# Performance work log

Measured on AMD Instinct MI355X. Metric: run time of the kernel, lower is better.

The kernel has to match this reference:

```python
import jax, jax.numpy as jnp
import numpy as np

B, T, F, H, O = 8192, 10, 561, 256, 12


def _lstm_cell(x, h, c, Wih, Whh, bih, bhh):
    # PyTorch gate order: input, forget, cell(g), output
    gates = x @ Wih.T + bih + h @ Whh.T + bhh  # [B, 4H]
    i, f, g, o = jnp.split(gates, 4, axis=-1)
    c_new = jax.nn.sigmoid(f) * c + jax.nn.sigmoid(i) * jnp.tanh(g)
    h_new = jax.nn.sigmoid(o) * jnp.tanh(c_new)
    return h_new, c_new


def setup_inputs() -> dict:
    key = jax.random.key(0)
    ks = jax.random.split(key, 12)
    s_in = 1.0 / np.sqrt(F)
    s_h = 1.0 / np.sqrt(H)
    u = lambda k, shape, s: jax.random.uniform(k, shape, jnp.float32, -s, s)
    return {
        "inputs": jax.random.normal(ks[0], (B, T, F), jnp.float32),
        "W_inp": u(ks[1], (H, F), s_in), "b_inp": u(ks[2], (H,), s_in),
        "Wih0": u(ks[3], (4 * H, H), s_h), "Whh0": u(ks[4], (4 * H, H), s_h),
        "bih0": u(ks[5], (4 * H,), s_h), "bhh0": u(ks[6], (4 * H,), s_h),
        "Wih1": u(ks[7], (4 * H, H), s_h), "Whh1": u(ks[8], (4 * H, H), s_h),
        "bih1": u(ks[9], (4 * H,), s_h), "bhh1": u(ks[10], (4 * H,), s_h),
        "W_out": u(ks[11], (O, H), s_h), "b_out": jnp.zeros((O,), jnp.float32),
    }


def reference(inputs, W_inp, b_inp, Wih0, Whh0, bih0, bhh0,
              Wih1, Whh1, bih1, bhh1, W_out, b_out):
    b, t, _ = inputs.shape
    h = W_inp.shape[0]
    # input Linear applied to every timestep (same math as per-step self.inp)
    xp = jnp.einsum('btf,hf->bth', inputs, W_inp) + b_inp  # [B,T,H]

    def step(carry, x_t):
        h0, c0, h1, c1 = carry
        h0, c0 = _lstm_cell(x_t, h0, c0, Wih0, Whh0, bih0, bhh0)
        h1, c1 = _lstm_cell(h0, h1, c1, Wih1, Whh1, bih1, bhh1)
        return (h0, c0, h1, c1), h1

    z = jnp.zeros((b, h), inputs.dtype)
    (h0, c0, h1, c1), hs = jax.lax.scan(step, (z, z, z, z), jnp.swapaxes(xp, 0, 1))
    outputs = jnp.einsum('tbh,oh->bto', hs, W_out) + b_out  # [B,T,O]
    h_n = jnp.stack([h0, h1])  # [2,B,H] like torch LSTM hidden
    c_n = jnp.stack([c0, c1])
    return outputs, h_n, c_n
```

## Files before the change

kernel.cpp:

```cpp
#include <hip/hip_runtime.h>

#define BB 8192
#define TT 10
#define FF 561
#define FP 576
#define HH 256
#define OO 12

typedef __attribute__((ext_vector_type(8))) __bf16 bf16x8;
typedef __attribute__((ext_vector_type(4))) float f32x4;

__device__ __forceinline__ unsigned short f2bf(float f) {
  unsigned int u = __float_as_uint(f);
  u += 0x7fffu + ((u >> 16) & 1u);
  return (unsigned short)(u >> 16);
}
__device__ __forceinline__ float bf2f(unsigned short s) {
  return __uint_as_float(((unsigned int)s) << 16);
}
__device__ __forceinline__ float sigm(float x) { return 1.f / (1.f + __expf(-x)); }
__device__ __forceinline__ float tanh_fast(float x) { return 1.f - 2.f / (__expf(2.f * x) + 1.f); }

__device__ __forceinline__ void gl_lds16(const unsigned short* g, unsigned short* l) {
  __builtin_amdgcn_global_load_lds(
      (const __attribute__((address_space(1))) unsigned int*)g,
      (__attribute__((address_space(3))) unsigned int*)l, 16, 0, 0);
}

__global__ void conv_inputs(const float* __restrict__ in, unsigned short* __restrict__ Ain) {
  int idx = blockIdx.x * 256 + threadIdx.x;
  if (idx >= 81920 * 144) return;
  int c4 = (idx % 144) * 4;
  size_t row = idx / 144;
  const float* src = in + row * 561 + c4;
  ushort4 v;
  v.x = f2bf(c4 + 0 < 561 ? src[0] : 0.f);
  v.y = f2bf(c4 + 1 < 561 ? src[1] : 0.f);
  v.z = f2bf(c4 + 2 < 561 ? src[2] : 0.f);
  v.w = f2bf(c4 + 3 < 561 ? src[3] : 0.f);
  *(ushort4*)(Ain + row * 576 + c4) = v;
}

__global__ void conv_weights(const float* __restrict__ Winp,
                             const float* __restrict__ Wih0, const float* __restrict__ Whh0,
                             const float* __restrict__ Wih1, const float* __restrict__ Whh1,
                             const float* __restrict__ Wout,
                             unsigned short* __restrict__ Wib,
                             unsigned short* __restrict__ W0p,
                             unsigned short* __restrict__ W1p,
                             unsigned short* __restrict__ Wob) {
  int idx = blockIdx.x * 256 + threadIdx.x;
  if (idx < 256 * 576) {
    int kk = idx % 576, n = idx / 576;
    Wib[idx] = f2bf(kk < 561 ? Winp[n * 561 + kk] : 0.f);
    return;
  }
  idx -= 256 * 576;
  if (idx < 1024 * 512) {
    int kk = idx % 512, np = idx / 512;
    int h = (np >> 7) * 32 + (np & 31), g = (np >> 5) & 3;
    int sr = g * 256 + h;
    float v = kk < 256 ? Wih0[sr * 256 + kk] : Whh0[sr * 256 + kk - 256];
    W0p[idx] = f2bf(v);
    return;
  }
  idx -= 1024 * 512;
  if (idx < 1024 * 512) {
    int kk = idx % 512, np = idx / 512;
    int h = (np >> 7) * 32 + (np & 31), g = (np >> 5) & 3;
    int sr = g * 256 + h;
    float v = kk < 256 ? Wih1[sr * 256 + kk] : Whh1[sr * 256 + kk - 256];
    W1p[idx] = f2bf(v);
    return;
  }
  idx -= 1024 * 512;
  if (idx < 16 * 256) {
    int kk = idx % 256, o = idx / 256;
    Wob[idx] = f2bf(o < OO ? Wout[o * 256 + kk] : 0.f);
  }
}

template <int MODE>
__global__ __launch_bounds__(256, 2) void gemm_k(
    const unsigned short* __restrict__ A0, int lda0, int K0,
    const unsigned short* __restrict__ A1, int lda1,
    const unsigned short* __restrict__ W, int K,
    const float* __restrict__ biasA, const float* __restrict__ biasB,
    float* __restrict__ cbuf,
    unsigned short* __restrict__ hout,
    float* __restrict__ hf32, float* __restrict__ cf32) {
  __shared__ __align__(16) unsigned short As[2][128 * 32];
  __shared__ __align__(16) unsigned short Bs[2][128 * 32];
  const int tid = threadIdx.x;
  const int w = tid >> 6, lane = tid & 63, quad = lane >> 4, l15 = lane & 15;
  const int mb = blockIdx.x, nb = blockIdx.y;

  f32x4 acc[2][8];
#pragma unroll
  for (int i = 0; i < 2; ++i)
#pragma unroll
    for (int j = 0; j < 8; ++j) acc[i][j] = (f32x4){0.f, 0.f, 0.f, 0.f};

  const int r0 = tid >> 2;
  const int cc = (tid & 3) * 8;

  auto stage = [&](int k0, int buf) {
    const unsigned short* Asrc;
    int ldA, kk;
    if (k0 < K0) { Asrc = A0; ldA = lda0; kk = k0; }
    else         { Asrc = A1; ldA = lda1; kk = k0 - K0; }
    gl_lds16(Asrc + (size_t)(mb * 128 + r0) * ldA + kk + cc, &As[buf][tid * 8]);
    gl_lds16(Asrc + (size_t)(mb * 128 + 64 + r0) * ldA + kk + cc, &As[buf][2048 + tid * 8]);
    gl_lds16(W + (size_t)(nb * 128 + r0) * K + k0 + cc, &Bs[buf][tid * 8]);
    gl_lds16(W + (size_t)(nb * 128 + 64 + r0) * K + k0 + cc, &Bs[buf][2048 + tid * 8]);
  };

  stage(0, 0);
  __syncthreads();

  int p = 0;
  for (int k0 = 0; k0 < K; k0 += 32) {
    if (k0 + 32 < K) stage(k0 + 32, p ^ 1);

    bf16x8 af[2], bfr[8];
#pragma unroll
    for (int mt = 0; mt < 2; ++mt)
      af[mt] = *(const bf16x8*)&As[p][(w * 32 + mt * 16 + l15) * 32 + quad * 8];
#pragma unroll
    for (int nt = 0; nt < 8; ++nt)
      bfr[nt] = *(const bf16x8*)&Bs[p][(nt * 16 + l15) * 32 + quad * 8];
#pragma unroll
    for (int mt = 0; mt < 2; ++mt)
#pragma unroll
      for (int nt = 0; nt < 8; ++nt)
        acc[mt][nt] = __builtin_amdgcn_mfma_f32_16x16x32_bf16(af[mt], bfr[nt], acc[mt][nt], 0, 0, 0);

    __syncthreads();
    p ^= 1;
  }

  if constexpr (MODE == 0) {
#pragma unroll
    for (int mt = 0; mt < 2; ++mt) {
      int rowb = mb * 128 + w * 32 + mt * 16 + quad * 4;
#pragma unroll
      for (int nt = 0; nt < 8; ++nt) {
        int col = nb * 128 + nt * 16 + l15;
        float bv = biasA[col];
#pragma unroll
        for (int r = 0; r < 4; ++r)
          hout[(size_t)(rowb + r) * HH + col] = f2bf(acc[mt][nt][r] + bv);
      }
    }
  } else {
#pragma unroll
    for (int hb = 0; hb < 2; ++hb) {
      int hg = nb * 32 + hb * 16 + l15;
      float bI = biasA[hg] + biasB[hg];
      float bF = biasA[256 + hg] + biasB[256 + hg];
      float bG = biasA[512 + hg] + biasB[512 + hg];
      float bO = biasA[768 + hg] + biasB[768 + hg];
#pragma unroll
      for (int mt = 0; mt < 2; ++mt) {
        int rowb = mb * 128 + w * 32 + mt * 16 + quad * 4;
#pragma unroll
        for (int r = 0; r < 4; ++r) {
          size_t idx = (size_t)(rowb + r) * HH + hg;
          float xi = acc[mt][0 + hb][r] + bI;
          float xf = acc[mt][2 + hb][r] + bF;
          float xg = acc[mt][4 + hb][r] + bG;
          float xo = acc[mt][6 + hb][r] + bO;
          float c_old = cbuf[idx];
          float cn = sigm(xf) * c_old + sigm(xi) * tanh_fast(xg);
          float hn = sigm(xo) * tanh_fast(cn);
          cbuf[idx] = cn;
          hout[idx] = f2bf(hn);
          if (hf32) hf32[idx] = hn;
          if (cf32) cf32[idx] = cn;
        }
      }
    }
  }
}

__global__ __launch_bounds__(256) void out_gemm_mfma(
    const unsigned short* __restrict__ hs,
    const unsigned short* __restrict__ Wob,
    const float* __restrict__ bout,
    float* __restrict__ out) {
  const int tid = threadIdx.x;
  const int w = tid >> 6, lane = tid & 63, quad = lane >> 4, l15 = lane & 15;
  const int m0 = blockIdx.x * 64 + w * 16;
  const unsigned short* arow = hs + (size_t)(m0 + l15 + BB) * HH + quad * 8;
  const unsigned short* brow = Wob + l15 * HH + quad * 8;
  f32x4 acc = (f32x4){0.f, 0.f, 0.f, 0.f};
#pragma unroll
  for (int k0 = 0; k0 < 8; ++k0) {
    bf16x8 a = *(const bf16x8*)(arow + k0 * 32);
    bf16x8 b = *(const bf16x8*)(brow + k0 * 32);
    acc = __builtin_amdgcn_mfma_f32_16x16x32_bf16(a, b, acc, 0, 0, 0);
  }
  const int o = l15;
  if (o < OO) {
    float bv = bout[o];
#pragma unroll
    for (int r = 0; r < 4; ++r) {
      int m = m0 + quad * 4 + r;
      int b = m & (BB - 1);
      int t = m >> 13;
      out[((size_t)b * TT + t) * OO + o] = acc[r] + bv;
    }
  }
}

extern "C" void kernel_launch(void* const* d_in, const int* in_sizes, int n_in,
                              void* d_out, int out_size, void* d_ws, size_t ws_size,
                              hipStream_t stream) {
  const float* inputs = (const float*)d_in[0];
  const float* W_inp  = (const float*)d_in[1];
  const float* b_inp  = (const float*)d_in[2];
  const float* Wih0   = (const float*)d_in[3];
  const float* Whh0   = (const float*)d_in[4];
  const float* bih0   = (const float*)d_in[5];
  const float* bhh0   = (const float*)d_in[6];
  const float* Wih1   = (const float*)d_in[7];
  const float* Whh1   = (const float*)d_in[8];
  const float* bih1   = (const float*)d_in[9];
  const float* bhh1   = (const float*)d_in[10];
  const float* W_out  = (const float*)d_in[11];
  const float* b_out  = (const float*)d_in[12];
  float* out = (float*)d_out;

  char* ws = (char*)d_ws;
  size_t off = 0;
  auto alloc = [&](size_t bytes) {
    char* p = ws + off;
    off += (bytes + 255) & ~(size_t)255;
    return p;
  };
  unsigned short* Ain = (unsigned short*)alloc((size_t)81920 * FP * 2);
  unsigned short* xp  = (unsigned short*)alloc((size_t)81920 * HH * 2);
  unsigned short* Wib = (unsigned short*)alloc((size_t)256 * FP * 2);
  unsigned short* W0p = (unsigned short*)alloc((size_t)1024 * 512 * 2);
  unsigned short* W1p = (unsigned short*)alloc((size_t)1024 * 512 * 2);
  unsigned short* Wob = (unsigned short*)alloc((size_t)16 * HH * 2);
  unsigned short* h0s = (unsigned short*)alloc((size_t)2 * BB * HH * 2);
  unsigned short* hs  = (unsigned short*)alloc((size_t)(TT + 1) * BB * HH * 2);
  float* c0 = (float*)alloc((size_t)BB * HH * 4);
  float* c1 = (float*)alloc((size_t)BB * HH * 4);

  hipMemsetAsync(h0s, 0, (size_t)BB * HH * 2, stream);
  hipMemsetAsync(hs, 0, (size_t)BB * HH * 2, stream);
  hipMemsetAsync(c0, 0, (size_t)BB * HH * 4, stream);
  hipMemsetAsync(c1, 0, (size_t)BB * HH * 4, stream);

  conv_inputs<<<(81920 * 144 + 255) / 256, 256, 0, stream>>>(inputs, Ain);
  {
    int nthr = 256 * 576 + 2 * 1024 * 512 + 16 * 256;
    conv_weights<<<(nthr + 255) / 256, 256, 0, stream>>>(W_inp, Wih0, Whh0, Wih1, Whh1,
                                                         W_out, Wib, W0p, W1p, Wob);
  }

  gemm_k<0><<<dim3(640, 2), 256, 0, stream>>>(
      Ain, FP, FP, (const unsigned short*)nullptr, 0,
      Wib, FP, b_inp, (const float*)nullptr,
      (float*)nullptr, xp, (float*)nullptr, (float*)nullptr);

  float* hn_out = out + (size_t)BB * TT * OO;
  float* cn_out = hn_out + (size_t)2 * BB * HH;

  for (int t = 0; t < TT; ++t) {
    const unsigned short* h0_prev = h0s + (size_t)(t & 1) * BB * HH;
    unsigned short* h0_new       = h0s + (size_t)((t + 1) & 1) * BB * HH;
    const unsigned short* xpt = xp + (size_t)t * HH;
    const unsigned short* h1_prev = hs + (size_t)t * BB * HH;
    unsigned short* h1_new        = hs + (size_t)(t + 1) * BB * HH;
    bool last = (t == TT - 1);

    gemm_k<1><<<dim3(64, 8), 256, 0, stream>>>(
        xpt, TT * HH, 256, h0_prev, HH,
        W0p, 512, bih0, bhh0, c0, h0_new,
        last ? hn_out : (float*)nullptr,
        last ? cn_out : (float*)nullptr);

    gemm_k<1><<<dim3(64, 8), 256, 0, stream>>>(
        h0_new, HH, 256, h1_prev, HH,
        W1p, 512, bih1, bhh1, c1, h1_new,
        last ? hn_out + (size_t)BB * HH : (float*)nullptr,
        last ? cn_out + (size_t)BB * HH : (float*)nullptr);
  }

  out_gemm_mfma<<<1280, 256, 0, stream>>>(hs, Wob, b_out, out);
}
```

Baseline: 790.8 us.

## Fuse LSTM recurrence into persistent cooperative kernel with wavefront layer pipelining

Replaces the 20 per-timestep GEMM launches with a single cooperative persistent kernel of 256 blocks. Half the blocks run layer 0 and half run layer 1, skewed by one step so both layers compute concurrently, with a grid sync between phases. The input projection now reads fp32 inputs directly through LDS and converts them to bf16 in registers, which removes the separate conversion kernel and its padded bf16 buffer. Tiles grow to 256x256 with 512 threads. The risks are grid-sync overhead, occupancy limits for cooperative launch, and the larger fp32 A tile in LDS.

```diff
diff --git a/kernel.cpp b/kernel.cpp
--- a/kernel.cpp
+++ b/kernel.cpp
@@ -1,4 +1,7 @@
 #include <hip/hip_runtime.h>
+#include <hip/hip_cooperative_groups.h>
+
+namespace cg = cooperative_groups;
 
 #define BB 8192
 #define TT 10
@@ -15,9 +18,6 @@
   u += 0x7fffu + ((u >> 16) & 1u);
   return (unsigned short)(u >> 16);
 }
-__device__ __forceinline__ float bf2f(unsigned short s) {
-  return __uint_as_float(((unsigned int)s) << 16);
-}
 __device__ __forceinline__ float sigm(float x) { return 1.f / (1.f + __expf(-x)); }
 __device__ __forceinline__ float tanh_fast(float x) { return 1.f - 2.f / (__expf(2.f * x) + 1.f); }
 
@@ -26,19 +26,19 @@
       (const __attribute__((address_space(1))) unsigned int*)g,
       (__attribute__((address_space(3))) unsigned int*)l, 16, 0, 0);
 }
-
-__global__ void conv_inputs(const float* __restrict__ in, unsigned short* __restrict__ Ain) {
-  int idx = blockIdx.x * 256 + threadIdx.x;
-  if (idx >= 81920 * 144) return;
-  int c4 = (idx % 144) * 4;
-  size_t row = idx / 144;
-  const float* src = in + row * 561 + c4;
-  ushort4 v;
-  v.x = f2bf(c4 + 0 < 561 ? src[0] : 0.f);
-  v.y = f2bf(c4 + 1 < 561 ? src[1] : 0.f);
-  v.z = f2bf(c4 + 2 < 561 ? src[2] : 0.f);
-  v.w = f2bf(c4 + 3 < 561 ? src[3] : 0.f);
-  *(ushort4*)(Ain + row * 576 + c4) = v;
+__device__ __forceinline__ void gl_lds4(const float* g, float* l) {
+  __builtin_amdgcn_global_load_lds(
+      (const __attribute__((address_space(1))) unsigned int*)g,
+      (__attribute__((address_space(3))) unsigned int*)l, 4, 0, 0);
+}
+
+__device__ __forceinline__ bf16x8 cvt8(const float* fp) {
+  f32x4 x0 = *(const f32x4*)fp;
+  f32x4 x1 = *(const f32x4*)(fp + 4);
+  union { bf16x8 v; unsigned short s[8]; } u;
+  u.s[0] = f2bf(x0[0]); u.s[1] = f2bf(x0[1]); u.s[2] = f2bf(x0[2]); u.s[3] = f2bf(x0[3]);
+  u.s[4] = f2bf(x1[0]); u.s[5] = f2bf(x1[1]); u.s[6] = f2bf(x1[2]); u.s[7] = f2bf(x1[3]);
+  return u.v;
 }
 
 __global__ void conv_weights(const float* __restrict__ Winp,
@@ -80,105 +80,193 @@
   }
 }
 
-template <int MODE>
-__global__ __launch_bounds__(256, 2) void gemm_k(
-    const unsigned short* __restrict__ A0, int lda0, int K0,
-    const unsigned short* __restrict__ A1, int lda1,
-    const unsigned short* __restrict__ W, int K,
-    const float* __restrict__ biasA, const float* __restrict__ biasB,
-    float* __restrict__ cbuf,
-    unsigned short* __restrict__ hout,
-    float* __restrict__ hf32, float* __restrict__ cf32) {
-  __shared__ __align__(16) unsigned short As[2][128 * 32];
-  __shared__ __align__(16) unsigned short Bs[2][128 * 32];
+__global__ __launch_bounds__(512, 2) void xp_gemm(
+    const float* __restrict__ in,
+    const unsigned short* __restrict__ Wib,
+    const float* __restrict__ binp,
+    unsigned short* __restrict__ xp) {
+  __shared__ __align__(16) float Af[2][128 * 32];
+  __shared__ __align__(16) unsigned short Bs[2][256 * 32];
   const int tid = threadIdx.x;
   const int w = tid >> 6, lane = tid & 63, quad = lane >> 4, l15 = lane & 15;
-  const int mb = blockIdx.x, nb = blockIdx.y;
+  const int wr = w & 3, wc = w >> 2;
+  const int mb = blockIdx.x;
+  const int ar = tid >> 5, acl = tid & 31;
+  const int sr = tid >> 2, sc = (tid & 3) * 8;
+
+  auto stage = [&](int k0, int buf) {
+#pragma unroll
+    for (int ii = 0; ii < 8; ++ii) {
+      int row = mb * 128 + ii * 16 + ar;
+      int col = k0 + acl; col = col < FF ? col : FF - 1;
+      gl_lds4(in + (size_t)row * FF + col, &Af[buf][(ii * 16 + ar) * 32 + acl]);
+    }
+    const unsigned short* g1 = Wib + (size_t)sr * FP + k0 + sc;
+    gl_lds16(g1, &Bs[buf][tid * 8]);
+    gl_lds16(g1 + (size_t)128 * FP, &Bs[buf][4096 + tid * 8]);
+  };
 
   f32x4 acc[2][8];
 #pragma unroll
   for (int i = 0; i < 2; ++i)
 #pragma unroll
     for (int j = 0; j < 8; ++j) acc[i][j] = (f32x4){0.f, 0.f, 0.f, 0.f};
-
-  const int r0 = tid >> 2;
-  const int cc = (tid & 3) * 8;
-
-  auto stage = [&](int k0, int buf) {
-    const unsigned short* Asrc;
-    int ldA, kk;
-    if (k0 < K0) { Asrc = A0; ldA = lda0; kk = k0; }
-    else         { Asrc = A1; ldA = lda1; kk = k0 - K0; }
-    gl_lds16(Asrc + (size_t)(mb * 128 + r0) * ldA + kk + cc, &As[buf][tid * 8]);
-    gl_lds16(Asrc + (size_t)(mb * 128 + 64 + r0) * ldA + kk + cc, &As[buf][2048 + tid * 8]);
-    gl_lds16(W + (size_t)(nb * 128 + r0) * K + k0 + cc, &Bs[buf][tid * 8]);
-    gl_lds16(W + (size_t)(nb * 128 + 64 + r0) * K + k0 + cc, &Bs[buf][2048 + tid * 8]);
-  };
 
   stage(0, 0);
   __syncthreads();
-
-  int p = 0;
-  for (int k0 = 0; k0 < K; k0 += 32) {
-    if (k0 + 32 < K) stage(k0 + 32, p ^ 1);
-
+  int pb = 0;
+  for (int k0 = 0; k0 < FP; k0 += 32) {
+    if (k0 + 32 < FP) stage(k0 + 32, pb ^ 1);
     bf16x8 af[2], bfr[8];
 #pragma unroll
     for (int mt = 0; mt < 2; ++mt)
-      af[mt] = *(const bf16x8*)&As[p][(w * 32 + mt * 16 + l15) * 32 + quad * 8];
+      af[mt] = cvt8(&Af[pb][(wr * 32 + mt * 16 + l15) * 32 + quad * 8]);
 #pragma unroll
     for (int nt = 0; nt < 8; ++nt)
-      bfr[nt] = *(const bf16x8*)&Bs[p][(nt * 16 + l15) * 32 + quad * 8];
+      bfr[nt] = *(const bf16x8*)&Bs[pb][(wc * 128 + nt * 16 + l15) * 32 + quad * 8];
 #pragma unroll
     for (int mt = 0; mt < 2; ++mt)
 #pragma unroll
       for (int nt = 0; nt < 8; ++nt)
         acc[mt][nt] = __builtin_amdgcn_mfma_f32_16x16x32_bf16(af[mt], bfr[nt], acc[mt][nt], 0, 0, 0);
-
     __syncthreads();
-    p ^= 1;
-  }
-
-  if constexpr (MODE == 0) {
-#pragma unroll
-    for (int mt = 0; mt < 2; ++mt) {
-      int rowb = mb * 128 + w * 32 + mt * 16 + quad * 4;
-#pragma unroll
-      for (int nt = 0; nt < 8; ++nt) {
-        int col = nb * 128 + nt * 16 + l15;
-        float bv = biasA[col];
-#pragma unroll
-        for (int r = 0; r < 4; ++r)
-          hout[(size_t)(rowb + r) * HH + col] = f2bf(acc[mt][nt][r] + bv);
+    pb ^= 1;
+  }
+
+#pragma unroll
+  for (int mt = 0; mt < 2; ++mt) {
+    int rowb = mb * 128 + wr * 32 + mt * 16 + quad * 4;
+#pragma unroll
+    for (int nt = 0; nt < 8; ++nt) {
+      int col = wc * 128 + nt * 16 + l15;
+      float bv = binp[col];
+#pragma unroll
+      for (int r = 0; r < 4; ++r)
+        xp[(size_t)(rowb + r) * HH + col] = f2bf(acc[mt][nt][r] + bv);
+    }
+  }
+}
+
+__global__ __launch_bounds__(512, 2) void lstm_recurrence(
+    const unsigned short* __restrict__ xp,
+    const unsigned short* __restrict__ W0p,
+    const unsigned short* __restrict__ W1p,
+    const float* __restrict__ bih0, const float* __restrict__ bhh0,
+    const float* __restrict__ bih1, const float* __restrict__ bhh1,
+    unsigned short* __restrict__ h0s,
+    unsigned short* __restrict__ hs,
+    float* __restrict__ c0, float* __restrict__ c1,
+    float* __restrict__ hn_out, float* __restrict__ cn_out) {
+  __shared__ __align__(16) unsigned short As[2][256 * 32];
+  __shared__ __align__(16) unsigned short Bs[2][256 * 32];
+  cg::grid_group gg = cg::this_grid();
+
+  const int tid = threadIdx.x;
+  const int w = tid >> 6, lane = tid & 63, quad = lane >> 4, l15 = lane & 15;
+  const int wr = w & 3, wc = w >> 2;
+  const int i = blockIdx.x;
+  const int xcd = i & 7, slot = i >> 3;
+  const int group = xcd >> 2;
+  const int mb = (xcd & 3) * 8 + (slot >> 2);
+  const int nb = slot & 3;
+
+  const unsigned short* W = group ? W1p : W0p;
+  const float* bA = group ? bih1 : bih0;
+  const float* bB = group ? bhh1 : bhh0;
+  float* cbuf = group ? c1 : c0;
+
+  const int sr = tid >> 2, sc = (tid & 3) * 8;
+
+  for (int p = 0; p <= TT; ++p) {
+    const bool active = group ? (p >= 1) : (p < TT);
+    if (active) {
+      const int t = group ? p - 1 : p;
+      const unsigned short* A0;
+      int lda0;
+      if (group) { A0 = h0s + (size_t)(p & 1) * BB * HH; lda0 = HH; }
+      else       { A0 = xp + (size_t)t * HH;             lda0 = TT * HH; }
+      const unsigned short* A1 = group ? (hs + (size_t)t * BB * HH)
+                                       : (h0s + (size_t)(p & 1) * BB * HH);
+
+      auto stageA = [&](int k0, int buf) {
+        const unsigned short* Asrc;
+        int ldA, kk;
+        if (k0 < 256) { Asrc = A0; ldA = lda0; kk = k0; }
+        else          { Asrc = A1; ldA = HH;   kk = k0 - 256; }
+        const unsigned short* g0 = Asrc + (size_t)(mb * 256 + sr) * ldA + kk + sc;
+        gl_lds16(g0, &As[buf][tid * 8]);
+        gl_lds16(g0 + (size_t)128 * ldA, &As[buf][4096 + tid * 8]);
+        const unsigned short* g1 = W + (size_t)(nb * 256 + sr) * 512 + k0 + sc;
+        gl_lds16(g1, &Bs[buf][tid * 8]);
+        gl_lds16(g1 + (size_t)128 * 512, &Bs[buf][4096 + tid * 8]);
+      };
+
+      f32x4 acc[4][8];
+#pragma unroll
+      for (int a = 0; a < 4; ++a)
+#pragma unroll
+        for (int b = 0; b < 8; ++b) acc[a][b] = (f32x4){0.f, 0.f, 0.f, 0.f};
+
+      stageA(0, 0);
+      __syncthreads();
+      int pb = 0;
+      for (int k0 = 0; k0 < 512; k0 += 32) {
+        if (k0 + 32 < 512) stageA(k0 + 32, pb ^ 1);
+        bf16x8 af[4], bfr[8];
+#pragma unroll
+        for (int mt = 0; mt < 4; ++mt)
+          af[mt] = *(const bf16x8*)&As[pb][(wr * 64 + mt * 16 + l15) * 32 + quad * 8];
+#pragma unroll
+        for (int nt = 0; nt < 8; ++nt)
+          bfr[nt] = *(const bf16x8*)&Bs[pb][(wc * 128 + nt * 16 + l15) * 32 + quad * 8];
+#pragma unroll
+        for (int mt = 0; mt < 4; ++mt)
+#pragma unroll
+          for (int nt = 0; nt < 8; ++nt)
+            acc[mt][nt] = __builtin_amdgcn_mfma_f32_16x16x32_bf16(af[mt], bfr[nt], acc[mt][nt], 0, 0, 0);
+        __syncthreads();
+        pb ^= 1;
       }
-    }
-  } else {
-#pragma unroll
-    for (int hb = 0; hb < 2; ++hb) {
-      int hg = nb * 32 + hb * 16 + l15;
-      float bI = biasA[hg] + biasB[hg];
-      float bF = biasA[256 + hg] + biasB[256 + hg];
-      float bG = biasA[512 + hg] + biasB[512 + hg];
-      float bO = biasA[768 + hg] + biasB[768 + hg];
-#pragma unroll
-      for (int mt = 0; mt < 2; ++mt) {
-        int rowb = mb * 128 + w * 32 + mt * 16 + quad * 4;
-#pragma unroll
-        for (int r = 0; r < 4; ++r) {
-          size_t idx = (size_t)(rowb + r) * HH + hg;
-          float xi = acc[mt][0 + hb][r] + bI;
-          float xf = acc[mt][2 + hb][r] + bF;
-          float xg = acc[mt][4 + hb][r] + bG;
-          float xo = acc[mt][6 + hb][r] + bO;
-          float c_old = cbuf[idx];
-          float cn = sigm(xf) * c_old + sigm(xi) * tanh_fast(xg);
-          float hn = sigm(xo) * tanh_fast(cn);
-          cbuf[idx] = cn;
-          hout[idx] = f2bf(hn);
-          if (hf32) hf32[idx] = hn;
-          if (cf32) cf32[idx] = cn;
+
+      unsigned short* hout = group ? (hs + (size_t)(t + 1) * BB * HH)
+                                   : (h0s + (size_t)((p + 1) & 1) * BB * HH);
+      float* hf = nullptr; float* cf = nullptr;
+      if (t == TT - 1) {
+        hf = hn_out + (group ? (size_t)BB * HH : 0);
+        cf = cn_out + (group ? (size_t)BB * HH : 0);
+      }
+      const int hg32 = (2 * nb + wc) * 32;
+#pragma unroll
+      for (int hb = 0; hb < 2; ++hb) {
+        const int hgl = hg32 + hb * 16 + l15;
+        float bI = bA[hgl] + bB[hgl];
+        float bF = bA[256 + hgl] + bB[256 + hgl];
+        float bG = bA[512 + hgl] + bB[512 + hgl];
+        float bO = bA[768 + hgl] + bB[768 + hgl];
+#pragma unroll
+        for (int mt = 0; mt < 4; ++mt) {
+          const int rowb = mb * 256 + wr * 64 + mt * 16 + quad * 4;
+#pragma unroll
+          for (int r = 0; r < 4; ++r) {
+            const size_t idx = (size_t)(rowb + r) * HH + hgl;
+            float xi = acc[mt][0 + hb][r] + bI;
+            float xf = acc[mt][2 + hb][r] + bF;
+            float xg = acc[mt][4 + hb][r] + bG;
+            float xo = acc[mt][6 + hb][r] + bO;
+            float c_old = cbuf[idx];
+            float cn = sigm(xf) * c_old + sigm(xi) * tanh_fast(xg);
+            float hn = sigm(xo) * tanh_fast(cn);
+            cbuf[idx] = cn;
+            hout[idx] = f2bf(hn);
+            if (hf) hf[idx] = hn;
+            if (cf) cf[idx] = cn;
+          }
         }
       }
+    }
+    if (p < TT) {
+      __threadfence();
+      gg.sync();
     }
   }
 }
@@ -238,7 +326,6 @@
     off += (bytes + 255) & ~(size_t)255;
     return p;
   };
-  unsigned short* Ain = (unsigned short*)alloc((size_t)81920 * FP * 2);
   unsigned short* xp  = (unsigned short*)alloc((size_t)81920 * HH * 2);
   unsigned short* Wib = (unsigned short*)alloc((size_t)256 * FP * 2);
   unsigned short* W0p = (unsigned short*)alloc((size_t)1024 * 512 * 2);
@@ -254,40 +341,24 @@
   hipMemsetAsync(c0, 0, (size_t)BB * HH * 4, stream);
   hipMemsetAsync(c1, 0, (size_t)BB * HH * 4, stream);
 
-  conv_inputs<<<(81920 * 144 + 255) / 256, 256, 0, stream>>>(inputs, Ain);
   {
     int nthr = 256 * 576 + 2 * 1024 * 512 + 16 * 256;
     conv_weights<<<(nthr + 255) / 256, 256, 0, stream>>>(W_inp, Wih0, Whh0, Wih1, Whh1,
                                                          W_out, Wib, W0p, W1p, Wob);
   }
 
-  gemm_k<0><<<dim3(640, 2), 256, 0, stream>>>(
-      Ain, FP, FP, (const unsigned short*)nullptr, 0,
-      Wib, FP, b_inp, (const float*)nullptr,
-      (float*)nullptr, xp, (float*)nullptr, (float*)nullptr);
+  xp_gemm<<<640, 512, 0, stream>>>(inputs, Wib, b_inp, xp);
 
   float* hn_out = out + (size_t)BB * TT * OO;
   float* cn_out = hn_out + (size_t)2 * BB * HH;
 
-  for (int t = 0; t < TT; ++t) {
-    const unsigned short* h0_prev = h0s + (size_t)(t & 1) * BB * HH;
-    unsigned short* h0_new       = h0s + (size_t)((t + 1) & 1) * BB * HH;
-    const unsigned short* xpt = xp + (size_t)t * HH;
-    const unsigned short* h1_prev = hs + (size_t)t * BB * HH;
-    unsigned short* h1_new        = hs + (size_t)(t + 1) * BB * HH;
-    bool last = (t == TT - 1);
-
-    gemm_k<1><<<dim3(64, 8), 256, 0, stream>>>(
-        xpt, TT * HH, 256, h0_prev, HH,
-        W0p, 512, bih0, bhh0, c0, h0_new,
-        last ? hn_out : (float*)nullptr,
-        last ? cn_out : (float*)nullptr);
-
-    gemm_k<1><<<dim3(64, 8), 256, 0, stream>>>(
-        h0_new, HH, 256, h1_prev, HH,
-        W1p, 512, bih1, bhh1, c1, h1_new,
-        last ? hn_out + (size_t)BB * HH : (float*)nullptr,
-        last ? cn_out + (size_t)BB * HH : (float*)nullptr);
+  {
+    void* args[] = {(void*)&xp, (void*)&W0p, (void*)&W1p,
+                    (void*)&bih0, (void*)&bhh0, (void*)&bih1, (void*)&bhh1,
+                    (void*)&h0s, (void*)&hs, (void*)&c0, (void*)&c1,
+                    (void*)&hn_out, (void*)&cn_out};
+    hipLaunchCooperativeKernel((void*)lstm_recurrence, dim3(256), dim3(512),
+                               args, 0, stream);
   }
 
   out_gemm_mfma<<<1280, 256, 0, stream>>>(hs, Wob, b_out, out);
```

Measured after the change: 1.707 ms. 2.16x slower.
